# Optimization experiments

Measured on AMD Instinct MI355X. Metric: run time of the kernel, lower is better.

## Reference

```python
import jax, jax.numpy as jnp
import numpy as np

B, S, H, M, E = 64, 512, 1024, 26, 676  # batch, seq, hidden, max_nodes, max_edges (M*M)


def setup_inputs() -> dict:
    key = jax.random.key(0)
    ks = jax.random.split(key, 16)
    seq = jax.random.normal(ks[0], (B, S, H), jnp.float32)
    # ragged, strictly-increasing sentence-end offsets in [1, S-1], zero-padded tail
    rng = np.random.RandomState(0)
    off = np.zeros((B, M - 1), np.int64)
    for b in range(B):
        c = rng.randint(5, M)  # count of valid offsets per sample (ragged)
        off[b, :c] = np.sort(rng.choice(np.arange(1, S), size=c, replace=False))
    s = 1.0 / np.sqrt(H)
    s3 = 1.0 / np.sqrt(3 * H)
    return {
        'sequence_outputs': seq,
        'proof_offsets': jnp.asarray(off),
        'node_labels': jax.random.randint(ks[1], (B, M), 0, 2),
        'edge_labels': jax.random.randint(ks[2], (B, E), 0, 2),
        'W_naf': jax.random.normal(ks[3], (H, H), jnp.float32) * s,
        'b_naf': jnp.zeros((H,), jnp.float32),
        'W_cd': jax.random.normal(ks[4], (H, H), jnp.float32) * s,
        'b_cd': jnp.zeros((H,), jnp.float32),
        'W_co': jax.random.normal(ks[5], (H, 2), jnp.float32) * s,
        'b_co': jnp.zeros((2,), jnp.float32),
        'W_nd': jax.random.normal(ks[6], (H, H), jnp.float32) * s,
        'b_nd': jnp.zeros((H,), jnp.float32),
        'W_no': jax.random.normal(ks[7], (H, 2), jnp.float32) * s,
        'b_no': jnp.zeros((2,), jnp.float32),
        'W_ed': jax.random.normal(ks[8], (3 * H, H), jnp.float32) * s3,
        'b_ed': jnp.zeros((H,), jnp.float32),
        'W_eo': jax.random.normal(ks[9], (H, 2), jnp.float32) * s,
        'b_eo': jnp.zeros((2,), jnp.float32),
    }


def reference(sequence_outputs, proof_offsets, node_labels, edge_labels,
              W_naf, b_naf, W_cd, b_cd, W_co, b_co,
              W_nd, b_nd, W_no, b_no, W_ed, b_ed, W_eo, b_eo):
    Bx, Sx, Hx = sequence_outputs.shape
    Mx = node_labels.shape[1]
    Ex = edge_labels.shape[1]

    cls = sequence_outputs[:, 0, :]                       # [B,H]
    naf = cls @ W_naf + b_naf                             # NAF node embedding
    logits = jnp.tanh(cls @ W_cd + b_cd) @ W_co + b_co    # RobertaClassificationHead (eval: dropout=id)

    # segment-mean pooling via inclusive prefix sums: segment j = tokens (prev_j, off_j]
    P = jnp.cumsum(sequence_outputs, axis=1)              # [B,S,H]
    off = proof_offsets                                   # [B,M-1]
    prev = jnp.concatenate([jnp.zeros((Bx, 1), off.dtype), off[:, :-1]], axis=1)
    valid = off > 0                                       # [B,M-1]
    seg_sum = (jnp.take_along_axis(P, off[..., None], axis=1)
               - jnp.take_along_axis(P, prev[..., None], axis=1))  # [B,M-1,H]
    seg_len = jnp.maximum(off - prev, 1).astype(sequence_outputs.dtype)
    seg_mean = seg_sum / seg_len[..., None] * valid[..., None]

    count = valid.sum(axis=1)                             # nodes per sample (excl. NAF)
    # node embeddings: seg means at 0..count-1, NAF at index count, zeros after
    node_full = jnp.concatenate([seg_mean, jnp.zeros((Bx, 1, Hx), seg_mean.dtype)], axis=1)  # [B,M,H]
    idx = jnp.arange(Mx)
    node_full = node_full + (idx[None, :, None] == count[:, None, None]) * naf[:, None, :]

    # all-pairs edge features over n=count+1 nodes, row-major flat k=i*n+j, zero-padded to E
    n = count + 1                                         # [B]
    k = jnp.arange(Ex)                                    # [E]
    i = jnp.clip(k[None, :] // n[:, None], 0, Mx - 1)     # [B,E]
    j = jnp.clip(k[None, :] % n[:, None], 0, Mx - 1)
    valid_e = (k[None, :] < (n * n)[:, None])[..., None]
    ni = jnp.take_along_axis(node_full, i[..., None], axis=1)  # [B,E,H]
    nj = jnp.take_along_axis(node_full, j[..., None], axis=1)
    edge = jnp.concatenate([nj, ni, nj - ni], axis=-1) * valid_e  # [B,E,3H]

    node_logits = jnp.tanh(node_full @ W_nd + b_nd) @ W_no + b_no
    edge_logits = jnp.tanh(edge @ W_ed + b_ed) @ W_eo + b_eo
    return (logits, node_logits, edge_logits)
```

## Files before the change

### kernel.cpp

```cpp
#include <hip/hip_runtime.h>
#include <hip/hip_bf16.h>

#define B_ 64
#define S_ 512
#define H_ 1024
#define M_ 26
#define E_ 676

typedef short bf16x8 __attribute__((ext_vector_type(8)));
typedef float f32x4 __attribute__((ext_vector_type(4)));

__device__ __forceinline__ void gload16(const void* g, void* l) {
    __builtin_amdgcn_global_load_lds((const __attribute__((address_space(1))) unsigned int*)g,
                                     (__attribute__((address_space(3))) unsigned int*)l,
                                     16, 0, 0);
}

__device__ __forceinline__ float tanh_fast(float x) {
    float e = __expf(2.0f * x);
    return 1.0f - 2.0f * __builtin_amdgcn_rcpf(e + 1.0f);
}

__global__ __launch_bounds__(256) void k_segmm(
    const float* __restrict__ seq, const int* __restrict__ off,
    __hip_bfloat16* __restrict__ nodeB) {
    __shared__ __hip_bfloat16 selL[32][520];
    __shared__ __hip_bfloat16 ldsB[2][256][40];
    __shared__ int offs_s[28];
    __shared__ float invL[32];
    int tid = threadIdx.x;
    int bid = blockIdx.x;
    int b = bid >> 2, h0 = (bid & 3) * 256;
    int w = tid >> 6, l = tid & 63;

    if (tid < M_ - 1) offs_s[tid] = off[b * (M_ - 1) + tid];
    __syncthreads();
    int c = 0;
    while (c < M_ - 1 && offs_s[c] > 0) c++;
    int offmax = offs_s[c - 1];

    {
        unsigned* p = (unsigned*)&selL[0][0];
        const int tot = 32 * 520 * 2 / 4;
        for (int i = tid; i < tot; i += 256) p[i] = 0u;
    }
    if (tid < 32)
        invL[tid] = (tid < c) ? 1.0f / (float)(offs_s[tid] - (tid ? offs_s[tid - 1] : 0))
                              : 0.0f;
    __syncthreads();
    for (int t = tid; t < 512; t += 256) {
        if (t >= 1 && t <= offmax) {
            int ms = 0;
            while (ms < c && offs_s[ms] < t) ms++;
            if (ms < c) *(unsigned short*)&selL[ms][t] = 0x3F80;
        }
    }
    __syncthreads();

    int nkt = (offmax >> 5) + 1;
    const float* sb = seq + (size_t)b * S_ * H_ + h0;
    float4 rg[8];
#pragma unroll
    for (int i = 0; i < 2; ++i)
#pragma unroll
        for (int r = 0; r < 4; ++r) {
            int tl = (i * 4 + w) * 4 + r;
            rg[i * 4 + r] = *(const float4*)(sb + (size_t)tl * H_ + 4 * l);
        }
    f32x4 acc[2][4] = {};

    for (int kt = 0; kt < nkt; ++kt) {
        asm volatile("s_waitcnt vmcnt(0)" ::: "memory");
        ushort4 pk[2][4];
#pragma unroll
        for (int i = 0; i < 2; ++i)
#pragma unroll
            for (int q = 0; q < 4; ++q) {
                float f0 = (q==0)?rg[i*4+0].x:(q==1)?rg[i*4+0].y:(q==2)?rg[i*4+0].z:rg[i*4+0].w;
                float f1 = (q==0)?rg[i*4+1].x:(q==1)?rg[i*4+1].y:(q==2)?rg[i*4+1].z:rg[i*4+1].w;
                float f2 = (q==0)?rg[i*4+2].x:(q==1)?rg[i*4+2].y:(q==2)?rg[i*4+2].z:rg[i*4+2].w;
                float f3 = (q==0)?rg[i*4+3].x:(q==1)?rg[i*4+3].y:(q==2)?rg[i*4+3].z:rg[i*4+3].w;
                __hip_bfloat16 __attribute__((aligned(8))) hh[4] = {
                    __float2bfloat16(f0), __float2bfloat16(f1),
                    __float2bfloat16(f2), __float2bfloat16(f3)};
                pk[i][q] = *(const ushort4*)hh;
            }
        if (kt + 1 < nkt) {
#pragma unroll
            for (int i = 0; i < 2; ++i)
#pragma unroll
                for (int r = 0; r < 4; ++r) {
                    int tl = (kt + 1) * 32 + (i * 4 + w) * 4 + r;
                    rg[i * 4 + r] = *(const float4*)(sb + (size_t)tl * H_ + 4 * l);
                }
            __builtin_amdgcn_sched_barrier(0);
        }
#pragma unroll
        for (int i = 0; i < 2; ++i)
#pragma unroll
            for (int q = 0; q < 4; ++q) {
                int hl = 4 * l + q;
                int tb = i * 4 + w;
                *(ushort4*)&ldsB[kt & 1][hl][tb * 4] = pk[i][q];
            }
        asm volatile("s_waitcnt lgkmcnt(0)" ::: "memory");
        __builtin_amdgcn_s_barrier();
        int T0 = kt * 32;
#pragma unroll
        for (int mt = 0; mt < 2; ++mt) {
            bf16x8 af = *(const bf16x8*)&selL[mt * 16 + (l & 15)][T0 + (l >> 4) * 8];
#pragma unroll
            for (int nn = 0; nn < 4; ++nn) {
                bf16x8 bfr = *(const bf16x8*)&ldsB[kt & 1][(w * 4 + nn) * 16 + (l & 15)]
                                                  [(l >> 4) * 8];
                acc[mt][nn] = __builtin_amdgcn_mfma_f32_16x16x32_bf16(af, bfr,
                                                                      acc[mt][nn], 0, 0, 0);
            }
        }
    }
#pragma unroll
    for (int mt = 0; mt < 2; ++mt)
#pragma unroll
        for (int nn = 0; nn < 4; ++nn) {
            f32x4 v = acc[mt][nn];
            int hcol = h0 + (w * 4 + nn) * 16 + (l & 15);
#pragma unroll
            for (int r = 0; r < 4; ++r) {
                int m = mt * 16 + (l >> 4) * 4 + r;
                if (m < M_)
                    nodeB[((size_t)(b * M_ + m)) * H_ + hcol] =
                        __float2bfloat16(v[r] * invL[m]);
            }
        }
}

__global__ __launch_bounds__(256) void k_stage1b(
    const float* __restrict__ seq, const int* __restrict__ off,
    const float* __restrict__ Wnaf, const float* __restrict__ Wcd,
    const float* __restrict__ Wnd, const float* __restrict__ Wed,
    const float* __restrict__ bed, const float* __restrict__ Weo,
    const float* __restrict__ beo,
    __hip_bfloat16* __restrict__ Wt, int* __restrict__ count,
    float* __restrict__ econ, float* __restrict__ naf, float* __restrict__ cdh) {
    __shared__ float smem[2048];
    int bid = blockIdx.x;
    int tid = threadIdx.x;

    if (bid < 256) {
        float (*As)[64] = (float(*)[64])smem;
        float (*Bs)[64] = (float(*)[64])(smem + 1024);
        int bx = bid & 31;
        int kbase = (bid >> 5) * 128;
        const float* W;
        float* dst;
        int cbase;
        if (bx < 16) { W = Wnaf; dst = naf; cbase = bx * 64; }
        else         { W = Wcd;  dst = cdh; cbase = (bx - 16) * 64; }
        int tx = tid % 16, ty = tid / 16;
        float c[4][4] = {};
        int la_row = tid / 4;
        int la_k4  = (tid % 4) * 4;
        int lb_k   = tid / 16;
        int lb_c4  = (tid % 16) * 4;
        for (int k0 = 0; k0 < 128; k0 += 16) {
            float4 a = *(const float4*)(seq + (size_t)la_row * S_ * H_ + kbase + k0 + la_k4);
            *(float4*)(&Bs[lb_k][lb_c4]) =
                *(const float4*)(W + (size_t)(kbase + k0 + lb_k) * H_ + cbase + lb_c4);
            As[la_k4 + 0][la_row] = a.x;
            As[la_k4 + 1][la_row] = a.y;
            As[la_k4 + 2][la_row] = a.z;
            As[la_k4 + 3][la_row] = a.w;
            __syncthreads();
#pragma unroll
            for (int kk = 0; kk < 16; ++kk) {
                float4 av = *(const float4*)(&As[kk][ty * 4]);
                float4 bv = *(const float4*)(&Bs[kk][tx * 4]);
                c[0][0] += av.x * bv.x; c[0][1] += av.x * bv.y; c[0][2] += av.x * bv.z; c[0][3] += av.x * bv.w;
                c[1][0] += av.y * bv.x; c[1][1] += av.y * bv.y; c[1][2] += av.y * bv.z; c[1][3] += av.y * bv.w;
                c[2][0] += av.z * bv.x; c[2][1] += av.z * bv.y; c[2][2] += av.z * bv.z; c[2][3] += av.z * bv.w;
                c[3][0] += av.w * bv.x; c[3][1] += av.w * bv.y; c[3][2] += av.w * bv.z; c[3][3] += av.w * bv.w;
            }
            __syncthreads();
        }
#pragma unroll
        for (int i = 0; i < 4; ++i)
#pragma unroll
            for (int j = 0; j < 4; ++j)
                atomicAdd(dst + (size_t)(ty * 4 + i) * H_ + cbase + tx * 4 + j, c[i][j]);
    } else if (bid < 3328) {
        float (*T)[33] = (float(*)[33])smem;
        int idx = bid - 256;
        int s = idx >> 10, rem = idx & 1023;
        int bx = rem & 31, by = rem >> 5;
        int c = tid & 31, r0 = tid >> 5;
        const int HH = H_ * H_;
#pragma unroll
        for (int i = 0; i < 4; ++i) {
            int r = r0 + 8 * i;
            size_t k = by * 32 + r, n = bx * 32 + c;
            float v;
            if (s == 0)      v = Wnd[k * H_ + n];
            else if (s == 1) v = Wed[k * H_ + n] + Wed[2 * HH + k * H_ + n];
            else             v = Wed[HH + k * H_ + n] - Wed[2 * HH + k * H_ + n];
            T[r][c] = v;
        }
        __syncthreads();
#pragma unroll
        for (int i = 0; i < 4; ++i) {
            int rr = r0 + 8 * i;
            Wt[(size_t)(s * H_ + bx * 32 + rr) * H_ + by * 32 + c] = __float2bfloat16(T[c][rr]);
        }
    } else if (bid == 3328) {
        if (tid < 64) {
            int b = tid;
            int c = 0;
            for (int m = 0; m < M_ - 1; ++m) c += (off[b * (M_ - 1) + m] > 0) ? 1 : 0;
            count[b] = c;
        }
    } else {
        float* s0 = smem; float* s1 = smem + 256;
        float a0 = 0.f, a1 = 0.f;
        for (int h = tid; h < H_; h += 256) {
            float t = tanh_fast(bed[h]);
            a0 += t * Weo[h * 2 + 0];
            a1 += t * Weo[h * 2 + 1];
        }
        s0[tid] = a0; s1[tid] = a1; __syncthreads();
        for (int o = 128; o > 0; o >>= 1) {
            if (tid < o) { s0[tid] += s0[tid + o]; s1[tid] += s1[tid + o]; }
            __syncthreads();
        }
        if (tid == 0) { econ[0] = s0[0] + beo[0]; econ[1] = s1[0] + beo[1]; }
    }
}

__global__ __launch_bounds__(256) void k_stage2s(
    const float* __restrict__ naf, const float* __restrict__ bnaf,
    const int* __restrict__ count, __hip_bfloat16* __restrict__ nodeB,
    const float* __restrict__ cdh, const float* __restrict__ bcd,
    const float* __restrict__ Wco, const float* __restrict__ bco,
    float* __restrict__ out) {
    __shared__ float smem[512];
    int bid = blockIdx.x;
    int tid = threadIdx.x;
    if (bid < 64) {
        int b = bid, cnt = count[b];
        float4 a = ((const float4*)(naf + (size_t)b * H_))[tid];
        float4 bb = ((const float4*)bnaf)[tid];
        __hip_bfloat16 __attribute__((aligned(8))) h[4] = {
            __float2bfloat16(a.x + bb.x), __float2bfloat16(a.y + bb.y),
            __float2bfloat16(a.z + bb.z), __float2bfloat16(a.w + bb.w)};
        *(ushort4*)(nodeB + ((size_t)(b * M_ + cnt)) * H_ + tid * 4) = *(const ushort4*)h;
    } else {
        int b = bid - 64;
        float* s0 = smem; float* s1 = smem + 256;
        float a0 = 0.f, a1 = 0.f;
        for (int h = tid; h < H_; h += 256) {
            float t = tanh_fast(cdh[(size_t)b * H_ + h] + bcd[h]);
            a0 += t * Wco[h * 2 + 0];
            a1 += t * Wco[h * 2 + 1];
        }
        s0[tid] = a0; s1[tid] = a1; __syncthreads();
        for (int o = 128; o > 0; o >>= 1) {
            if (tid < o) { s0[tid] += s0[tid + o]; s1[tid] += s1[tid + o]; }
            __syncthreads();
        }
        if (tid == 0) { out[b * 2 + 0] = s0[0] + bco[0]; out[b * 2 + 1] = s1[0] + bco[1]; }
    }
}

#define GM 1664
#define GN 3072
#define GK 1024
__global__ __launch_bounds__(256) void k_mfma(const __hip_bfloat16* __restrict__ A,
                                              const __hip_bfloat16* __restrict__ Bt,
                                              float* __restrict__ C) {
    __shared__ __hip_bfloat16 As[128 * 32];
    __shared__ __hip_bfloat16 Bs[128 * 32];
    int tid = threadIdx.x;
    int wid = tid >> 6, ln = tid & 63;
    int row0 = blockIdx.y * 128, col0 = blockIdx.x * 128;
    const __hip_bfloat16* ga = A + (size_t)(row0 + wid * 16 + (ln >> 2)) * GK + (ln & 3) * 8;
    const __hip_bfloat16* gb = Bt + (size_t)(col0 + wid * 16 + (ln >> 2)) * GK + (ln & 3) * 8;
    __hip_bfloat16* lA = As + wid * 512;
    __hip_bfloat16* lB = Bs + wid * 512;
    int mrow = (wid >> 1) * 64, ncol = (wid & 1) * 64;
    int l15 = ln & 15, l4 = ln >> 4;
    f32x4 acc[4][4] = {};
    const __hip_bfloat16* pa = As + (size_t)(mrow + l15) * 32 + l4 * 8;
    const __hip_bfloat16* pb = Bs + (size_t)(ncol + l15) * 32 + l4 * 8;
    for (int k0 = 0; k0 < GK; k0 += 32) {
        gload16(ga, lA);
        gload16(ga + 64 * GK, lA + 2048);
        gload16(gb, lB);
        gload16(gb + 64 * GK, lB + 2048);
        ga += 32; gb += 32;
        __syncthreads();
        bf16x8 af[4], bf[4];
#pragma unroll
        for (int mi = 0; mi < 4; ++mi) af[mi] = *(const bf16x8*)(pa + mi * 16 * 32);
#pragma unroll
        for (int ni = 0; ni < 4; ++ni) bf[ni] = *(const bf16x8*)(pb + ni * 16 * 32);
#pragma unroll
        for (int mi = 0; mi < 4; ++mi)
#pragma unroll
            for (int ni = 0; ni < 4; ++ni)
                acc[mi][ni] = __builtin_amdgcn_mfma_f32_16x16x32_bf16(af[mi], bf[ni],
                                                                      acc[mi][ni], 0, 0, 0);
        __syncthreads();
    }
#pragma unroll
    for (int mi = 0; mi < 4; ++mi)
#pragma unroll
        for (int ni = 0; ni < 4; ++ni) {
            f32x4 v = acc[mi][ni];
            size_t r = row0 + mrow + mi * 16 + l4 * 4;
            size_t cc = col0 + ncol + ni * 16 + l15;
            C[(r + 0) * GN + cc] = v[0];
            C[(r + 1) * GN + cc] = v[1];
            C[(r + 2) * GN + cc] = v[2];
            C[(r + 3) * GN + cc] = v[3];
        }
}

__global__ __launch_bounds__(256) void k_stage4(
    const float* __restrict__ Cm, const int* __restrict__ count,
    const float* __restrict__ bnd, const float* __restrict__ Wno,
    const float* __restrict__ bno, const float* __restrict__ bed,
    const float* __restrict__ Weo, const float* __restrict__ beo,
    const float* __restrict__ econ, float* __restrict__ out_n,
    float* __restrict__ out_e) {
    int bid = blockIdx.x;
    int wid = threadIdx.x >> 6, lane = threadIdx.x & 63;
    if (bid < 416) {
        int r = bid * 4 + wid;
        const float4* src = (const float4*)(Cm + (size_t)r * GN);
        float a0 = 0.f, a1 = 0.f;
#pragma unroll
        for (int it = 0; it < 4; ++it) {
            int h = lane * 4 + it * 256;
            float4 s = src[lane + it * 64];
            float4 bb = *(const float4*)(bnd + h);
            float t0 = tanh_fast(s.x + bb.x), t1 = tanh_fast(s.y + bb.y);
            float t2 = tanh_fast(s.z + bb.z), t3 = tanh_fast(s.w + bb.w);
            a0 += t0 * Wno[h * 2 + 0] + t1 * Wno[h * 2 + 2] + t2 * Wno[h * 2 + 4] + t3 * Wno[h * 2 + 6];
            a1 += t0 * Wno[h * 2 + 1] + t1 * Wno[h * 2 + 3] + t2 * Wno[h * 2 + 5] + t3 * Wno[h * 2 + 7];
        }
        for (int o = 32; o > 0; o >>= 1) { a0 += __shfl_down(a0, o); a1 += __shfl_down(a1, o); }
        if (lane == 0) { out_n[(size_t)r * 2 + 0] = a0 + bno[0]; out_n[(size_t)r * 2 + 1] = a1 + bno[1]; }
    } else {
        int e = bid - 416;
        int b = e >> 4;
        int wg = (e & 15) * 4 + wid;
        int n = count[b] + 1;
        int n2 = n * n;
        float4 bed4[4], w04[4], w14[4];
#pragma unroll
        for (int it = 0; it < 4; ++it) {
            int h = lane * 4 + it * 256;
            bed4[it] = *(const float4*)(bed + h);
            w04[it] = make_float4(Weo[h * 2 + 0], Weo[h * 2 + 2], Weo[h * 2 + 4], Weo[h * 2 + 6]);
            w14[it] = make_float4(Weo[h * 2 + 1], Weo[h * 2 + 3], Weo[h * 2 + 5], Weo[h * 2 + 7]);
        }
        float e0 = econ[0], e1 = econ[1];
        float b0 = beo[0], b1 = beo[1];
        for (int k = wg; k < E_; k += 64) {
            float* dst = out_e + ((size_t)b * E_ + k) * 2;
            if (k >= n2) {
                if (lane == 0) { dst[0] = e0; dst[1] = e1; }
                continue;
            }
            int i = k / n, j = k - i * n;
            const float4* U4 = (const float4*)(Cm + (size_t)(b * M_ + j) * GN + H_);
            const float4* V4 = (const float4*)(Cm + (size_t)(b * M_ + i) * GN + 2 * H_);
            float a0 = 0.f, a1 = 0.f;
#pragma unroll
            for (int it = 0; it < 4; ++it) {
                float4 u = U4[lane + it * 64];
                float4 v = V4[lane + it * 64];
                float t0 = tanh_fast(u.x + v.x + bed4[it].x);
                float t1 = tanh_fast(u.y + v.y + bed4[it].y);
                float t2 = tanh_fast(u.z + v.z + bed4[it].z);
                float t3 = tanh_fast(u.w + v.w + bed4[it].w);
                a0 += t0 * w04[it].x + t1 * w04[it].y + t2 * w04[it].z + t3 * w04[it].w;
                a1 += t0 * w14[it].x + t1 * w14[it].y + t2 * w14[it].z + t3 * w14[it].w;
            }
            for (int o = 32; o > 0; o >>= 1) { a0 += __shfl_down(a0, o); a1 += __shfl_down(a1, o); }
            if (lane == 0) { dst[0] = a0 + b0; dst[1] = a1 + b1; }
        }
    }
}

extern "C" void kernel_launch(void* const* d_in, const int* in_sizes, int n_in,
                              void* d_out, int out_size, void* d_ws, size_t ws_size,
                              hipStream_t stream) {
    const float* seq  = (const float*)d_in[0];
    const int*   off  = (const int*)d_in[1];
    const float* Wnaf = (const float*)d_in[4];  const float* bnaf = (const float*)d_in[5];
    const float* Wcd  = (const float*)d_in[6];  const float* bcd  = (const float*)d_in[7];
    const float* Wco  = (const float*)d_in[8];  const float* bco  = (const float*)d_in[9];
    const float* Wnd  = (const float*)d_in[10]; const float* bnd  = (const float*)d_in[11];
    const float* Wno  = (const float*)d_in[12]; const float* bno  = (const float*)d_in[13];
    const float* Wed  = (const float*)d_in[14]; const float* bed  = (const float*)d_in[15];
    const float* Weo  = (const float*)d_in[16]; const float* beo  = (const float*)d_in[17];
    float* out = (float*)d_out;

    float* ws = (float*)d_ws;
    size_t p = 0;
    float* naf   = ws + p;  p += (size_t)B_ * H_;
    float* cdh   = ws + p;  p += (size_t)B_ * H_;
    __hip_bfloat16* nodeB = (__hip_bfloat16*)(ws + p); p += (size_t)B_ * M_ * H_ / 2;
    __hip_bfloat16* Wt    = (__hip_bfloat16*)(ws + p); p += (size_t)3 * H_ * H_ / 2;
    float* Cbuf  = ws + p;  p += (size_t)GM * GN;
    int*   cnt   = (int*)(ws + p); p += 64;
    float* econ  = ws + p;  p += 2;

    hipMemsetAsync(naf, 0, 2 * (size_t)B_ * H_ * sizeof(float), stream);

    k_segmm<<<dim3(256), 256, 0, stream>>>(seq, off, nodeB);
    k_stage1b<<<dim3(3330), 256, 0, stream>>>(seq, off, Wnaf, Wcd, Wnd, Wed, bed, Weo, beo,
                                              Wt, cnt, econ, naf, cdh);
    k_stage2s<<<dim3(128), 256, 0, stream>>>(naf, bnaf, cnt, nodeB,
                                             cdh, bcd, Wco, bco, out);
    k_mfma<<<dim3(GN / 128, GM / 128), 256, 0, stream>>>(nodeB, Wt, Cbuf);
    k_stage4<<<dim3(1440), 256, 0, stream>>>(Cbuf, cnt, bnd, Wno, bno, bed, Weo, beo, econ,
                                             out + B_ * 2, out + B_ * 2 + B_ * M_ * 2);
}
```

Before: 317.8 us.

## Merge segment-mean kernel into stage-1 launch with register-generated selector

Folds the segment-mean MFMA kernel into the stage-1 multi-role kernel as the first 256 blocks, removing one launch and letting segment pooling overlap with the weight transpose and CLS GEMM blocks. The 0/1 selector matrix is no longer materialised in LDS. It is built in registers from per-row offset bounds, which cuts LDS use and the zero-fill pass. The LDS B tile goes from double- to single-buffered, with an extra barrier per k-step, so the shared LDS size fits all roles at the cost of more synchronisation.

```diff
diff --git a/kernel.cpp b/kernel.cpp
--- a/kernel.cpp
+++ b/kernel.cpp
@@ -21,136 +21,121 @@
     return 1.0f - 2.0f * __builtin_amdgcn_rcpf(e + 1.0f);
 }
 
-__global__ __launch_bounds__(256) void k_segmm(
-    const float* __restrict__ seq, const int* __restrict__ off,
-    __hip_bfloat16* __restrict__ nodeB) {
-    __shared__ __hip_bfloat16 selL[32][520];
-    __shared__ __hip_bfloat16 ldsB[2][256][40];
-    __shared__ int offs_s[28];
-    __shared__ float invL[32];
-    int tid = threadIdx.x;
-    int bid = blockIdx.x;
-    int b = bid >> 2, h0 = (bid & 3) * 256;
-    int w = tid >> 6, l = tid & 63;
-
-    if (tid < M_ - 1) offs_s[tid] = off[b * (M_ - 1) + tid];
-    __syncthreads();
-    int c = 0;
-    while (c < M_ - 1 && offs_s[c] > 0) c++;
-    int offmax = offs_s[c - 1];
-
-    {
-        unsigned* p = (unsigned*)&selL[0][0];
-        const int tot = 32 * 520 * 2 / 4;
-        for (int i = tid; i < tot; i += 256) p[i] = 0u;
-    }
-    if (tid < 32)
-        invL[tid] = (tid < c) ? 1.0f / (float)(offs_s[tid] - (tid ? offs_s[tid - 1] : 0))
-                              : 0.0f;
-    __syncthreads();
-    for (int t = tid; t < 512; t += 256) {
-        if (t >= 1 && t <= offmax) {
-            int ms = 0;
-            while (ms < c && offs_s[ms] < t) ms++;
-            if (ms < c) *(unsigned short*)&selL[ms][t] = 0x3F80;
-        }
-    }
-    __syncthreads();
-
-    int nkt = (offmax >> 5) + 1;
-    const float* sb = seq + (size_t)b * S_ * H_ + h0;
-    float4 rg[8];
-#pragma unroll
-    for (int i = 0; i < 2; ++i)
-#pragma unroll
-        for (int r = 0; r < 4; ++r) {
-            int tl = (i * 4 + w) * 4 + r;
-            rg[i * 4 + r] = *(const float4*)(sb + (size_t)tl * H_ + 4 * l);
-        }
-    f32x4 acc[2][4] = {};
-
-    for (int kt = 0; kt < nkt; ++kt) {
-        asm volatile("s_waitcnt vmcnt(0)" ::: "memory");
-        ushort4 pk[2][4];
-#pragma unroll
-        for (int i = 0; i < 2; ++i)
-#pragma unroll
-            for (int q = 0; q < 4; ++q) {
-                float f0 = (q==0)?rg[i*4+0].x:(q==1)?rg[i*4+0].y:(q==2)?rg[i*4+0].z:rg[i*4+0].w;
-                float f1 = (q==0)?rg[i*4+1].x:(q==1)?rg[i*4+1].y:(q==2)?rg[i*4+1].z:rg[i*4+1].w;
-                float f2 = (q==0)?rg[i*4+2].x:(q==1)?rg[i*4+2].y:(q==2)?rg[i*4+2].z:rg[i*4+2].w;
-                float f3 = (q==0)?rg[i*4+3].x:(q==1)?rg[i*4+3].y:(q==2)?rg[i*4+3].z:rg[i*4+3].w;
-                __hip_bfloat16 __attribute__((aligned(8))) hh[4] = {
-                    __float2bfloat16(f0), __float2bfloat16(f1),
-                    __float2bfloat16(f2), __float2bfloat16(f3)};
-                pk[i][q] = *(const ushort4*)hh;
-            }
-        if (kt + 1 < nkt) {
-#pragma unroll
-            for (int i = 0; i < 2; ++i)
-#pragma unroll
-                for (int r = 0; r < 4; ++r) {
-                    int tl = (kt + 1) * 32 + (i * 4 + w) * 4 + r;
-                    rg[i * 4 + r] = *(const float4*)(sb + (size_t)tl * H_ + 4 * l);
-                }
-            __builtin_amdgcn_sched_barrier(0);
-        }
-#pragma unroll
-        for (int i = 0; i < 2; ++i)
-#pragma unroll
-            for (int q = 0; q < 4; ++q) {
-                int hl = 4 * l + q;
-                int tb = i * 4 + w;
-                *(ushort4*)&ldsB[kt & 1][hl][tb * 4] = pk[i][q];
-            }
-        asm volatile("s_waitcnt lgkmcnt(0)" ::: "memory");
-        __builtin_amdgcn_s_barrier();
-        int T0 = kt * 32;
-#pragma unroll
-        for (int mt = 0; mt < 2; ++mt) {
-            bf16x8 af = *(const bf16x8*)&selL[mt * 16 + (l & 15)][T0 + (l >> 4) * 8];
-#pragma unroll
-            for (int nn = 0; nn < 4; ++nn) {
-                bf16x8 bfr = *(const bf16x8*)&ldsB[kt & 1][(w * 4 + nn) * 16 + (l & 15)]
-                                                  [(l >> 4) * 8];
-                acc[mt][nn] = __builtin_amdgcn_mfma_f32_16x16x32_bf16(af, bfr,
-                                                                      acc[mt][nn], 0, 0, 0);
-            }
-        }
-    }
-#pragma unroll
-    for (int mt = 0; mt < 2; ++mt)
-#pragma unroll
-        for (int nn = 0; nn < 4; ++nn) {
-            f32x4 v = acc[mt][nn];
-            int hcol = h0 + (w * 4 + nn) * 16 + (l & 15);
-#pragma unroll
-            for (int r = 0; r < 4; ++r) {
-                int m = mt * 16 + (l >> 4) * 4 + r;
-                if (m < M_)
-                    nodeB[((size_t)(b * M_ + m)) * H_ + hcol] =
-                        __float2bfloat16(v[r] * invL[m]);
-            }
-        }
-}
-
-__global__ __launch_bounds__(256) void k_stage1b(
+__global__ __launch_bounds__(256) void k_stage1(
     const float* __restrict__ seq, const int* __restrict__ off,
     const float* __restrict__ Wnaf, const float* __restrict__ Wcd,
     const float* __restrict__ Wnd, const float* __restrict__ Wed,
     const float* __restrict__ bed, const float* __restrict__ Weo,
     const float* __restrict__ beo,
     __hip_bfloat16* __restrict__ Wt, int* __restrict__ count,
-    float* __restrict__ econ, float* __restrict__ naf, float* __restrict__ cdh) {
-    __shared__ float smem[2048];
+    float* __restrict__ econ, float* __restrict__ naf, float* __restrict__ cdh,
+    __hip_bfloat16* __restrict__ nodeB) {
+    __shared__ __attribute__((aligned(16))) char smraw[20992];
     int bid = blockIdx.x;
     int tid = threadIdx.x;
 
     if (bid < 256) {
+        __hip_bfloat16 (*ldsB)[40] = (__hip_bfloat16(*)[40])smraw;
+        int* offs_s = (int*)(smraw + 20480);
+        float* invL = (float*)(smraw + 20608);
+        int b = bid >> 2, h0 = (bid & 3) * 256;
+        int w = tid >> 6, l = tid & 63;
+
+        if (tid < M_ - 1) offs_s[tid] = off[b * (M_ - 1) + tid];
+        __syncthreads();
+        int c = 0;
+        while (c < M_ - 1 && offs_s[c] > 0) c++;
+        int offmax = offs_s[c - 1];
+        if (tid < 32)
+            invL[tid] = (tid < c) ? 1.0f / (float)(offs_s[tid] - (tid ? offs_s[tid - 1] : 0))
+                                  : 0.0f;
+        int row0 = (l & 15), row1 = 16 + (l & 15);
+        int offm0 = (row0 < c) ? offs_s[row0] : 0;
+        int prv0  = (offm0 > 0) ? (row0 ? offs_s[row0 - 1] : 0) : 1;
+        int offm1 = (row1 < c) ? offs_s[row1] : 0;
+        int prv1  = (offm1 > 0) ? offs_s[row1 - 1] : 1;
+
+        int nkt = (offmax >> 5) + 1;
+        const float* sb = seq + (size_t)b * S_ * H_ + h0;
+        float4 rg[8];
+#pragma unroll
+        for (int i = 0; i < 2; ++i)
+#pragma unroll
+            for (int r = 0; r < 4; ++r)
+                rg[i * 4 + r] = *(const float4*)(sb + (size_t)((i * 4 + w) * 4 + r) * H_ + 4 * l);
+        f32x4 acc[2][4] = {};
+        int tA = (l >> 4) * 8;
+
+        for (int kt = 0; kt < nkt; ++kt) {
+            asm volatile("s_waitcnt vmcnt(0)" ::: "memory");
+            ushort4 pk[2][4];
+#pragma unroll
+            for (int i = 0; i < 2; ++i)
+#pragma unroll
+                for (int q = 0; q < 4; ++q) {
+                    float f0 = (q==0)?rg[i*4+0].x:(q==1)?rg[i*4+0].y:(q==2)?rg[i*4+0].z:rg[i*4+0].w;
+                    float f1 = (q==0)?rg[i*4+1].x:(q==1)?rg[i*4+1].y:(q==2)?rg[i*4+1].z:rg[i*4+1].w;
+                    float f2 = (q==0)?rg[i*4+2].x:(q==1)?rg[i*4+2].y:(q==2)?rg[i*4+2].z:rg[i*4+2].w;
+                    float f3 = (q==0)?rg[i*4+3].x:(q==1)?rg[i*4+3].y:(q==2)?rg[i*4+3].z:rg[i*4+3].w;
+                    __hip_bfloat16 __attribute__((aligned(8))) hh[4] = {
+                        __float2bfloat16(f0), __float2bfloat16(f1),
+                        __float2bfloat16(f2), __float2bfloat16(f3)};
+                    pk[i][q] = *(const ushort4*)hh;
+                }
+            if (kt + 1 < nkt) {
+#pragma unroll
+                for (int i = 0; i < 2; ++i)
+#pragma unroll
+                    for (int r = 0; r < 4; ++r) {
+                        int tl = (kt + 1) * 32 + (i * 4 + w) * 4 + r;
+                        rg[i * 4 + r] = *(const float4*)(sb + (size_t)tl * H_ + 4 * l);
+                    }
+                __builtin_amdgcn_sched_barrier(0);
+            }
+#pragma unroll
+            for (int i = 0; i < 2; ++i)
+#pragma unroll
+                for (int q = 0; q < 4; ++q)
+                    *(ushort4*)&ldsB[4 * l + q][(i * 4 + w) * 4] = pk[i][q];
+            asm volatile("s_waitcnt lgkmcnt(0)" ::: "memory");
+            __builtin_amdgcn_s_barrier();
+            int T0 = kt * 32;
+            bf16x8 af0, af1;
+#pragma unroll
+            for (int i = 0; i < 8; ++i) {
+                int t = T0 + tA + i;
+                af0[i] = (t > prv0 && t <= offm0) ? (short)0x3F80 : (short)0;
+                af1[i] = (t > prv1 && t <= offm1) ? (short)0x3F80 : (short)0;
+            }
+#pragma unroll
+            for (int nn = 0; nn < 4; ++nn) {
+                bf16x8 bfr = *(const bf16x8*)&ldsB[(w * 4 + nn) * 16 + (l & 15)][tA];
+                acc[0][nn] = __builtin_amdgcn_mfma_f32_16x16x32_bf16(af0, bfr, acc[0][nn], 0, 0, 0);
+                acc[1][nn] = __builtin_amdgcn_mfma_f32_16x16x32_bf16(af1, bfr, acc[1][nn], 0, 0, 0);
+            }
+            __builtin_amdgcn_s_barrier();
+        }
+#pragma unroll
+        for (int mt = 0; mt < 2; ++mt)
+#pragma unroll
+            for (int nn = 0; nn < 4; ++nn) {
+                f32x4 v = acc[mt][nn];
+                int hcol = h0 + (w * 4 + nn) * 16 + (l & 15);
+#pragma unroll
+                for (int r = 0; r < 4; ++r) {
+                    int m = mt * 16 + (l >> 4) * 4 + r;
+                    if (m < M_)
+                        nodeB[((size_t)(b * M_ + m)) * H_ + hcol] =
+                            __float2bfloat16(v[r] * invL[m]);
+                }
+            }
+    } else if (bid < 512) {
+        float* smem = (float*)smraw;
         float (*As)[64] = (float(*)[64])smem;
         float (*Bs)[64] = (float(*)[64])(smem + 1024);
-        int bx = bid & 31;
-        int kbase = (bid >> 5) * 128;
+        int e = bid - 256;
+        int bx = e & 31;
+        int kbase = (e >> 5) * 128;
         const float* W;
         float* dst;
         int cbase;
@@ -187,9 +172,9 @@
 #pragma unroll
             for (int j = 0; j < 4; ++j)
                 atomicAdd(dst + (size_t)(ty * 4 + i) * H_ + cbase + tx * 4 + j, c[i][j]);
-    } else if (bid < 3328) {
-        float (*T)[33] = (float(*)[33])smem;
-        int idx = bid - 256;
+    } else if (bid < 3584) {
+        float (*T)[33] = (float(*)[33])smraw;
+        int idx = bid - 512;
         int s = idx >> 10, rem = idx & 1023;
         int bx = rem & 31, by = rem >> 5;
         int c = tid & 31, r0 = tid >> 5;
@@ -210,7 +195,7 @@
             int rr = r0 + 8 * i;
             Wt[(size_t)(s * H_ + bx * 32 + rr) * H_ + by * 32 + c] = __float2bfloat16(T[c][rr]);
         }
-    } else if (bid == 3328) {
+    } else if (bid == 3584) {
         if (tid < 64) {
             int b = tid;
             int c = 0;
@@ -218,7 +203,7 @@
             count[b] = c;
         }
     } else {
-        float* s0 = smem; float* s1 = smem + 256;
+        float* s0 = (float*)smraw; float* s1 = (float*)smraw + 256;
         float a0 = 0.f, a1 = 0.f;
         for (int h = tid; h < H_; h += 256) {
             float t = tanh_fast(bed[h]);
@@ -417,9 +402,8 @@
 
     hipMemsetAsync(naf, 0, 2 * (size_t)B_ * H_ * sizeof(float), stream);
 
-    k_segmm<<<dim3(256), 256, 0, stream>>>(seq, off, nodeB);
-    k_stage1b<<<dim3(3330), 256, 0, stream>>>(seq, off, Wnaf, Wcd, Wnd, Wed, bed, Weo, beo,
-                                              Wt, cnt, econ, naf, cdh);
+    k_stage1<<<dim3(3586), 256, 0, stream>>>(seq, off, Wnaf, Wcd, Wnd, Wed, bed, Weo, beo,
+                                             Wt, cnt, econ, naf, cdh, nodeB);
     k_stage2s<<<dim3(128), 256, 0, stream>>>(naf, bnaf, cnt, nodeB,
                                              cdh, bcd, Wco, bco, out);
     k_mfma<<<dim3(GN / 128, GM / 128), 256, 0, stream>>>(nodeB, Wt, Cbuf);
```

Result: faster. 310.4 us (-2.3%).
